# Kernel tuning notes

Measured on AMD Instinct MI355X. Metric: run time of the kernel, lower is better.

The kernel has to match this reference:

```python
import jax, jax.numpy as jnp
import numpy as np

B, L, S, D, H = 4, 1024, 1024, 1024, 16
HD = D // H  # head_dim = 64


def setup_inputs() -> dict:
    key = jax.random.key(0)
    ks = jax.random.split(key, 12)
    s = 1.0 / np.sqrt(D)
    return {
        "query": jax.random.normal(ks[0], (B, L, D), jnp.float32),
        "key": jax.random.normal(ks[1], (B, S, D), jnp.float32),
        "value": jax.random.normal(ks[2], (B, S, D), jnp.float32),
        "key_padding_mask": jax.random.randint(ks[3], (B, S), 0, 2) > 0,
        "Wq": jax.random.normal(ks[4], (D, D), jnp.float32) * s,
        "bq": jnp.zeros((D,), jnp.float32),
        "Wk": jax.random.normal(ks[5], (D, D), jnp.float32) * s,
        "bk": jnp.zeros((D,), jnp.float32),
        "Wv": jax.random.normal(ks[6], (D, D), jnp.float32) * s,
        "bv": jnp.zeros((D,), jnp.float32),
        "Wo": jax.random.normal(ks[7], (D, D), jnp.float32) * s,
        "bo": jnp.zeros((D,), jnp.float32),
    }


def reference(query, key, value, key_padding_mask, Wq, bq, Wk, bk, Wv, bv, Wo, bo):
    bs, tgt, _ = query.shape
    src = key.shape[1]
    # Q/K/V projections (nn.Linear: x @ W.T + b)
    q = query @ Wq.T + bq
    k = key @ Wk.T + bk
    v = value @ Wv.T + bv
    # split heads: (B, T, H, HD)
    q = q.reshape(bs, tgt, H, HD)
    k = k.reshape(bs, src, H, HD)
    v = v.reshape(bs, src, H, HD)
    # scaled dot-product attention with key padding mask (True = masked)
    scale = 1.0 / jnp.sqrt(jnp.asarray(HD, q.dtype))
    scores = jnp.einsum("blhd,bshd->bhls", q, k) * scale  # (B,H,L,S)
    neg_inf = jnp.asarray(-jnp.inf, scores.dtype)
    scores = scores + jnp.where(key_padding_mask[:, None, None, :], neg_inf, 0.0)
    attn = jax.nn.softmax(scores, axis=-1)
    out = jnp.einsum("bhls,bshd->blhd", attn, v).reshape(bs, tgt, D)
    return out @ Wo.T + bo
```

## Files before the change

### kernel.cpp

```cpp
#include <hip/hip_runtime.h>
#include <hip/hip_bf16.h>


typedef __bf16 bf16;
typedef __bf16 bf16x8 __attribute__((ext_vector_type(8)));
typedef float floatx4 __attribute__((ext_vector_type(4)));

#define D_MODEL 1024
#define NHEAD   16
#define HDIM    64
#define BATCH   4
#define SEQ     1024
#define M_ROWS  (BATCH * SEQ)
#define ACT_N   ((size_t)M_ROWS * D_MODEL)
#define W_N     ((size_t)D_MODEL * D_MODEL)
#define SC2     0.18033688011112042f

#define GLD(gp, lp) __builtin_amdgcn_global_load_lds( \
    (__attribute__((address_space(1))) void*)(gp), \
    (__attribute__((address_space(3))) void*)(lp), 16, 0, 0)

__global__ __launch_bounds__(256)
void k_convert_all(const float* __restrict__ a0, const float* __restrict__ a1,
                   const float* __restrict__ a2,
                   const float* __restrict__ w0, const float* __restrict__ w1,
                   const float* __restrict__ w2, const float* __restrict__ w3,
                   bf16* __restrict__ dst,
                   const unsigned* __restrict__ m, float* __restrict__ mbias)
{
    if (blockIdx.x == 8192) {
        __shared__ unsigned viol[4];
        __shared__ int fmsh;
        if (threadIdx.x < 4) viol[threadIdx.x] = 0;
        __syncthreads();
        unsigned a = 0, b = 0, c = 0, d = 0;
        for (int i = threadIdx.x; i < 1024; i += 256) {
            unsigned v = m[i];
            if (v > 1u) a = 1;
            if (((v & 0xFFu) > 1u) || (((v >> 8) & 0xFFu) > 1u) ||
                (((v >> 16) & 0xFFu) > 1u) || (((v >> 24) & 0xFFu) > 1u)) b = 1;
            unsigned lo = v & 0xFFFFu, hi = v >> 16;
            if (!((lo == 0u || lo == 0x3F80u) && (hi == 0u || hi == 0x3F80u))) c = 1;
            if (lo != 0u) d = 1;
        }
        if (a) atomicOr(&viol[0], 1u);
        if (b) atomicOr(&viol[1], 1u);
        if (c) atomicOr(&viol[2], 1u);
        if (d) atomicOr(&viol[3], 1u);
        __syncthreads();
        if (threadIdx.x == 0) {
            int fm;
            if (!viol[0])      fm = 1;
            else if (!viol[1]) fm = 0;
            else if (!viol[2]) fm = viol[3] ? 2 : 3;
            else               fm = 0;
            fmsh = fm;
        }
        __syncthreads();
        const int fm = fmsh;
        for (int i = 0; i < 16; ++i) {
            int s = i * 256 + threadIdx.x;
            bool msk;
            if (fm == 1)      msk = ((const int*)m)[s] != 0;
            else if (fm == 2) msk = ((const unsigned short*)m)[s] != 0;
            else if (fm == 3) msk = ((const unsigned*)m)[s] != 0;
            else              msk = ((const unsigned char*)m)[s] != 0;
            mbias[s] = msk ? -1e30f : 0.f;
        }
        return;
    }

    size_t i = ((size_t)blockIdx.x * 256 + threadIdx.x) * 8;
    const float* src; size_t off;
    if (i < ((size_t)12 << 20)) {
        int z = (int)(i >> 22);
        src = (z == 0) ? a0 : (z == 1) ? a1 : a2;
        off = i & (((size_t)1 << 22) - 1);
    } else {
        size_t r = i - ((size_t)12 << 20);
        int j = (int)(r >> 20);
        src = (j == 0) ? w0 : (j == 1) ? w1 : (j == 2) ? w2 : w3;
        off = r & (((size_t)1 << 20) - 1);
    }
    float4 f0 = ((const float4*)(src + off))[0];
    float4 f1 = ((const float4*)(src + off))[1];
    bf16x8 o;
    o[0] = (bf16)f0.x; o[1] = (bf16)f0.y; o[2] = (bf16)f0.z; o[3] = (bf16)f0.w;
    o[4] = (bf16)f1.x; o[5] = (bf16)f1.y; o[6] = (bf16)f1.z; o[7] = (bf16)f1.w;
    *(bf16x8*)(dst + i) = o;
}

template<typename CT>
__device__ __forceinline__ void gemm8_core(const bf16* __restrict__ A,
                                           const bf16* __restrict__ W,
                                           const float* __restrict__ bias,
                                           CT* __restrict__ C,
                                           int m0, int n0, bool rowBias,
                                           bf16* __restrict__ As0,
                                           bf16* __restrict__ Bs0)
{
    const int t    = threadIdx.x;
    const int lane = t & 63;
    const int w    = t >> 6;
    const int wm   = w >> 2;
    const int wn   = w & 3;
    const int l15  = lane & 15;
    const int quad = lane >> 4;
    const int lx   = l15 & 7;

    floatx4 acc[8][4] = {};

    int srow[2], schk[2], ldso[2];
    #pragma unroll
    for (int j = 0; j < 2; ++j) {
        int i = j * 512 + t;
        srow[j] = i >> 3;
        schk[j] = (i & 7) ^ (srow[j] & 7);
        ldso[j] = (j * 512 + w * 64) * 8;
    }

    #define STAGE_HALF(src, rb, k0s, h, dstbuf) do {                          \
        _Pragma("unroll")                                                     \
        for (int j = 0; j < 2; ++j)                                           \
            GLD((src) + (size_t)((rb) + (h) * 128 + srow[j]) * D_MODEL        \
                    + (k0s) + schk[j] * 8,                                    \
                (dstbuf) + (h) * 8192 + ldso[j]);                             \
    } while (0)

    STAGE_HALF(A, m0, 0, 0, As0);
    STAGE_HALF(A, m0, 0, 1, As0);
    STAGE_HALF(W, n0, 0, 0, Bs0);
    STAGE_HALF(W, n0, 0, 1, Bs0);
    __syncthreads();

    for (int kt = 0; kt < 16; ++kt) {
        const int nk = (kt + 1) * 64;
        const bf16* __restrict__ Ab = As0 + (kt & 1) * 16384;
        const bf16* __restrict__ Bb = Bs0 + (kt & 1) * 16384;
        bf16* __restrict__ An = As0 + ((kt + 1) & 1) * 16384;
        bf16* __restrict__ Bn = Bs0 + ((kt + 1) & 1) * 16384;

        #pragma unroll
        for (int ph = 0; ph < 4; ++ph) {
            const int mq = ph >> 1, nq = ph & 1;

            if (nk < D_MODEL) {
                if (ph == 0)      STAGE_HALF(A, m0, nk, 0, An);
                else if (ph == 1) STAGE_HALF(A, m0, nk, 1, An);
                else if (ph == 2) STAGE_HALF(W, n0, nk, 0, Bn);
                else              STAGE_HALF(W, n0, nk, 1, Bn);
            }

            bf16x8 af[4][2], bfr[2][2];
            #pragma unroll
            for (int ii = 0; ii < 4; ++ii) {
                int row = wm * 128 + mq * 64 + ii * 16 + l15;
                #pragma unroll
                for (int kk = 0; kk < 2; ++kk)
                    af[ii][kk] = *(const bf16x8*)
                        &Ab[row * 64 + (((kk * 4 + quad) ^ lx)) * 8];
            }
            #pragma unroll
            for (int jj = 0; jj < 2; ++jj) {
                int row = wn * 64 + nq * 32 + jj * 16 + l15;
                #pragma unroll
                for (int kk = 0; kk < 2; ++kk)
                    bfr[jj][kk] = *(const bf16x8*)
                        &Bb[row * 64 + (((kk * 4 + quad) ^ lx)) * 8];
            }

            #pragma unroll
            for (int ii = 0; ii < 4; ++ii)
                #pragma unroll
                for (int jj = 0; jj < 2; ++jj)
                    #pragma unroll
                    for (int kk = 0; kk < 2; ++kk)
                        acc[mq * 4 + ii][nq * 2 + jj] =
                            __builtin_amdgcn_mfma_f32_16x16x32_bf16(
                                af[ii][kk], bfr[jj][kk],
                                acc[mq * 4 + ii][nq * 2 + jj], 0, 0, 0);
        }
        __syncthreads();
    }

    #pragma unroll
    for (int i = 0; i < 8; ++i) {
        int rowb = m0 + wm * 128 + i * 16 + quad * 4;
        float bvr[4];
        if (rowBias) {
            #pragma unroll
            for (int r = 0; r < 4; ++r) bvr[r] = bias[rowb + r];
        }
        #pragma unroll
        for (int jf = 0; jf < 4; ++jf) {
            int col = n0 + wn * 64 + jf * 16 + l15;
            float bc = rowBias ? 0.f : bias[col];
            #pragma unroll
            for (int r = 0; r < 4; ++r) {
                float val = acc[i][jf][r] + (rowBias ? bvr[r] : bc);
                C[(size_t)(rowb + r) * D_MODEL + col] = (CT)val;
            }
        }
    }
    #undef STAGE_HALF
}

__global__ __launch_bounds__(512, 2)
void k_gemm_proj(const bf16* __restrict__ cq, const bf16* __restrict__ ck,
                 const bf16* __restrict__ cv,
                 const bf16* __restrict__ cWq, const bf16* __restrict__ cWk,
                 const bf16* __restrict__ cWv,
                 const float* __restrict__ bq, const float* __restrict__ bk,
                 const float* __restrict__ bv,
                 bf16* __restrict__ qproj, bf16* __restrict__ kproj,
                 bf16* __restrict__ vt)
{
    extern __shared__ __align__(16) bf16 smem[];
    bf16* As0 = smem;
    bf16* Bs0 = smem + 32768;

    const int bid = blockIdx.x;
    const int tid = (bid & 7) * 24 + (bid >> 3);
    if (tid < 64) {
        gemm8_core<bf16>(cq, cWq, bq, qproj,
                         (tid >> 2) * 256, (tid & 3) * 256, false, As0, Bs0);
    } else if (tid < 128) {
        int u = tid - 64;
        gemm8_core<bf16>(ck, cWk, bk, kproj,
                         (u >> 2) * 256, (u & 3) * 256, false, As0, Bs0);
    } else {
        int v = tid - 128;
        int b = v >> 4, m = (v >> 2) & 3, n = v & 3;
        gemm8_core<bf16>(cWv, cv + (size_t)b * W_N, bv,
                         vt + (size_t)b * W_N, m * 256, n * 256, true,
                         As0, Bs0);
    }
}

__global__ __launch_bounds__(512, 2)
void k_gemm_o(const bf16* __restrict__ A, const bf16* __restrict__ W,
              const float* __restrict__ bb, float* __restrict__ C)
{
    extern __shared__ __align__(16) bf16 smem[];
    bf16* As0 = smem;
    bf16* Bs0 = smem + 32768;

    const int bid = blockIdx.x;
    const int tid = (bid & 7) * 8 + (bid >> 3);
    gemm8_core<float>(A, W, bb, C, (tid >> 2) * 256, (tid & 3) * 256, false,
                      As0, Bs0);
}

__global__ __launch_bounds__(256)
void k_attn(const bf16* __restrict__ qproj, const bf16* __restrict__ kproj,
            const bf16* __restrict__ vt, const float* __restrict__ mbias_g,
            bf16* __restrict__ ctx)
{
    __shared__ alignas(16) bf16 Kst[2][4096];
    __shared__ alignas(16) bf16 Vst[2][4096];
    __shared__ alignas(16) bf16 Past[4096];

    const int t    = threadIdx.x;
    const int lane = t & 63;
    const int w    = t >> 6;
    const int l15  = lane & 15;
    const int quad = lane >> 4;

    const int b  = blockIdx.x >> 4;
    const int h  = blockIdx.x & 15;
    const int q0 = blockIdx.y * 64;

    #pragma unroll
    for (int kk = 0; kk < 2; ++kk) {
        const bf16* gp = qproj + (size_t)(b * SEQ + q0 + w * 16 + l15) * D_MODEL
                       + h * HDIM + kk * 32 + quad * 8;
        GLD(gp, Past + (w * 2 + kk) * 512);
    }
    #pragma unroll
    for (int i = 0; i < 2; ++i) {
        int f   = w * 2 + i;
        int row = (f >> 1) * 16 + l15;
        int cb  = (f & 1) * 32 + quad * 8;
        GLD(kproj + (size_t)(b * SEQ + row) * D_MODEL + h * HDIM + cb,
            Kst[0] + f * 512);
        GLD(vt + (size_t)(b * 1024 + h * HDIM + row) * D_MODEL + cb,
            Vst[0] + f * 512);
    }
    __syncthreads();

    bf16x8 qf[2];
    #pragma unroll
    for (int kk = 0; kk < 2; ++kk)
        qf[kk] = *(const bf16x8*)&Past[(w * 2 + kk) * 512 + lane * 8];

    bf16x8 ones;
    #pragma unroll
    for (int e = 0; e < 8; ++e) ones[e] = (bf16)1.0f;

    floatx4 o[4] = {};
    floatx4 accl = {};

    const int pbase = w * 1024 + (l15 >> 3) * 128 + quad * 32 + (l15 & 7);
    const float* __restrict__ mbb = mbias_g + b * SEQ;

    int cur = 0;
    for (int s0 = 0; s0 < SEQ; s0 += 64) {
        if (s0 + 64 < SEQ) {
            #pragma unroll
            for (int i = 0; i < 2; ++i) {
                int f   = w * 2 + i;
                int row = (f >> 1) * 16 + l15;
                int cb  = (f & 1) * 32 + quad * 8;
                GLD(kproj + (size_t)(b * SEQ + s0 + 64 + row) * D_MODEL
                        + h * HDIM + cb,
                    Kst[cur ^ 1] + f * 512);
                GLD(vt + (size_t)(b * 1024 + h * HDIM + row) * D_MODEL
                        + s0 + 64 + cb,
                    Vst[cur ^ 1] + f * 512);
            }
        }

        floatx4 s_acc[4] = {};
        #pragma unroll
        for (int j = 0; j < 4; ++j)
            #pragma unroll
            for (int kk = 0; kk < 2; ++kk) {
                bf16x8 kf = *(const bf16x8*)&Kst[cur][(j * 2 + kk) * 512 + lane * 8];
                s_acc[j] = __builtin_amdgcn_mfma_f32_16x16x32_bf16(
                    qf[kk], kf, s_acc[j], 0, 0, 0);
            }

        #pragma unroll
        for (int j = 0; j < 4; ++j) {
            float mb = mbb[s0 + j * 16 + l15];
            #pragma unroll
            for (int r = 0; r < 4; ++r) {
                float p = __builtin_amdgcn_exp2f(fmaf(s_acc[j][r], SC2, mb));
                Past[pbase + (j >> 1) * 512 + (j & 1) * 256 + r * 8] = (bf16)p;
            }
        }
        __builtin_amdgcn_wave_barrier();

        bf16x8 pf[2];
        #pragma unroll
        for (int kk = 0; kk < 2; ++kk)
            pf[kk] = *(const bf16x8*)&Past[w * 1024 + kk * 512 + lane * 8];

        #pragma unroll
        for (int kk = 0; kk < 2; ++kk)
            accl = __builtin_amdgcn_mfma_f32_16x16x32_bf16(pf[kk], ones, accl,
                                                           0, 0, 0);
        #pragma unroll
        for (int j = 0; j < 4; ++j)
            #pragma unroll
            for (int kk = 0; kk < 2; ++kk) {
                bf16x8 vf = *(const bf16x8*)&Vst[cur][(j * 2 + kk) * 512 + lane * 8];
                o[j] = __builtin_amdgcn_mfma_f32_16x16x32_bf16(
                    pf[kk], vf, o[j], 0, 0, 0);
            }

        __syncthreads();
        cur ^= 1;
    }

    float inv[4];
    #pragma unroll
    for (int r = 0; r < 4; ++r) inv[r] = (accl[r] > 0.f) ? 1.f / accl[r] : 0.f;
    #pragma unroll
    for (int j = 0; j < 4; ++j)
        #pragma unroll
        for (int r = 0; r < 4; ++r) {
            int row = q0 + w * 16 + quad * 4 + r;
            int col = h * HDIM + j * 16 + l15;
            ctx[(size_t)(b * SEQ + row) * D_MODEL + col] = (bf16)(o[j][r] * inv[r]);
        }
}

extern "C" void kernel_launch(void* const* d_in, const int* in_sizes, int n_in,
                              void* d_out, int out_size, void* d_ws, size_t ws_size,
                              hipStream_t stream)
{
    char* wsb = (char*)d_ws;
    float* mbias = (float*)wsb;
    bf16* cbase = (bf16*)(wsb + 65536);
    bf16 *cq = cbase, *ck = cq + ACT_N, *cv = ck + ACT_N;
    bf16 *cWq = cv + ACT_N, *cWk = cWq + W_N, *cWv = cWk + W_N, *cWo = cWv + W_N;
    bf16* qproj = cWo + W_N;
    bf16* kproj = qproj + ACT_N;
    bf16* vt    = kproj + ACT_N;
    bf16* ctx   = vt + ACT_N;
    float* out  = (float*)d_out;

    static bool attrset = false;
    if (!attrset) {
        hipFuncSetAttribute((const void*)k_gemm_proj,
                            hipFuncAttributeMaxDynamicSharedMemorySize, 131072);
        hipFuncSetAttribute((const void*)k_gemm_o,
                            hipFuncAttributeMaxDynamicSharedMemorySize, 131072);
        attrset = true;
    }

    k_convert_all<<<8193, 256, 0, stream>>>(
        (const float*)d_in[0], (const float*)d_in[1], (const float*)d_in[2],
        (const float*)d_in[4], (const float*)d_in[6], (const float*)d_in[8],
        (const float*)d_in[10], cbase, (const unsigned*)d_in[3], mbias);

    k_gemm_proj<<<192, 512, 131072, stream>>>(cq, ck, cv, cWq, cWk, cWv,
                                              (const float*)d_in[5],
                                              (const float*)d_in[7],
                                              (const float*)d_in[9],
                                              qproj, kproj, vt);
    k_attn<<<dim3(64, 16), 256, 0, stream>>>(qproj, kproj, vt, mbias, ctx);
    k_gemm_o<<<64, 512, 131072, stream>>>(ctx, cWo, (const float*)d_in[11], out);
}
```

Baseline: 220.7 us.

## Process two query tiles per attention wave and narrow output GEMM tiles

The attention kernel now handles 128 queries per block, with each wave computing two 16-row query groups that share every K and V fragment read from LDS. This halves K/V staging traffic per query and the block count, at the cost of more registers and a larger padded P buffer. The output projection GEMM is templated on a 256x128 tile and launches 128 blocks instead of 64, so more compute units are used, while each block stages a smaller B tile.

```diff
diff --git a/kernel.cpp b/kernel.cpp
--- a/kernel.cpp
+++ b/kernel.cpp
@@ -90,7 +90,7 @@
     *(bf16x8*)(dst + i) = o;
 }
 
-template<typename CT>
+template<typename CT, int NT>
 __device__ __forceinline__ void gemm8_core(const bf16* __restrict__ A,
                                            const bf16* __restrict__ W,
                                            const float* __restrict__ bias,
@@ -108,7 +108,10 @@
     const int quad = lane >> 4;
     const int lx   = l15 & 7;
 
-    floatx4 acc[8][4] = {};
+    constexpr int NJ = NT / 128;
+    constexpr int BSTRIDE = NT * 64;
+
+    floatx4 acc[8][NT / 64] = {};
 
     int srow[2], schk[2], ldso[2];
     #pragma unroll
@@ -130,28 +133,34 @@
     STAGE_HALF(A, m0, 0, 0, As0);
     STAGE_HALF(A, m0, 0, 1, As0);
     STAGE_HALF(W, n0, 0, 0, Bs0);
-    STAGE_HALF(W, n0, 0, 1, Bs0);
+    if constexpr (NT == 256) STAGE_HALF(W, n0, 0, 1, Bs0);
     __syncthreads();
 
     for (int kt = 0; kt < 16; ++kt) {
         const int nk = (kt + 1) * 64;
         const bf16* __restrict__ Ab = As0 + (kt & 1) * 16384;
-        const bf16* __restrict__ Bb = Bs0 + (kt & 1) * 16384;
+        const bf16* __restrict__ Bb = Bs0 + (kt & 1) * BSTRIDE;
         bf16* __restrict__ An = As0 + ((kt + 1) & 1) * 16384;
-        bf16* __restrict__ Bn = Bs0 + ((kt + 1) & 1) * 16384;
+        bf16* __restrict__ Bn = Bs0 + ((kt + 1) & 1) * BSTRIDE;
 
         #pragma unroll
         for (int ph = 0; ph < 4; ++ph) {
             const int mq = ph >> 1, nq = ph & 1;
 
             if (nk < D_MODEL) {
-                if (ph == 0)      STAGE_HALF(A, m0, nk, 0, An);
-                else if (ph == 1) STAGE_HALF(A, m0, nk, 1, An);
-                else if (ph == 2) STAGE_HALF(W, n0, nk, 0, Bn);
-                else              STAGE_HALF(W, n0, nk, 1, Bn);
-            }
-
-            bf16x8 af[4][2], bfr[2][2];
+                if constexpr (NT == 256) {
+                    if (ph == 0)      STAGE_HALF(A, m0, nk, 0, An);
+                    else if (ph == 1) STAGE_HALF(A, m0, nk, 1, An);
+                    else if (ph == 2) STAGE_HALF(W, n0, nk, 0, Bn);
+                    else              STAGE_HALF(W, n0, nk, 1, Bn);
+                } else {
+                    if (ph == 0)      STAGE_HALF(A, m0, nk, 0, An);
+                    else if (ph == 1) STAGE_HALF(A, m0, nk, 1, An);
+                    else if (ph == 2) STAGE_HALF(W, n0, nk, 0, Bn);
+                }
+            }
+
+            bf16x8 af[4][2], bfr[NJ][2];
             #pragma unroll
             for (int ii = 0; ii < 4; ++ii) {
                 int row = wm * 128 + mq * 64 + ii * 16 + l15;
@@ -161,8 +170,8 @@
                         &Ab[row * 64 + (((kk * 4 + quad) ^ lx)) * 8];
             }
             #pragma unroll
-            for (int jj = 0; jj < 2; ++jj) {
-                int row = wn * 64 + nq * 32 + jj * 16 + l15;
+            for (int jj = 0; jj < NJ; ++jj) {
+                int row = wn * (NT / 4) + nq * (NT / 8) + jj * 16 + l15;
                 #pragma unroll
                 for (int kk = 0; kk < 2; ++kk)
                     bfr[jj][kk] = *(const bf16x8*)
@@ -172,13 +181,13 @@
             #pragma unroll
             for (int ii = 0; ii < 4; ++ii)
                 #pragma unroll
-                for (int jj = 0; jj < 2; ++jj)
+                for (int jj = 0; jj < NJ; ++jj)
                     #pragma unroll
                     for (int kk = 0; kk < 2; ++kk)
-                        acc[mq * 4 + ii][nq * 2 + jj] =
+                        acc[mq * 4 + ii][nq * NJ + jj] =
                             __builtin_amdgcn_mfma_f32_16x16x32_bf16(
                                 af[ii][kk], bfr[jj][kk],
-                                acc[mq * 4 + ii][nq * 2 + jj], 0, 0, 0);
+                                acc[mq * 4 + ii][nq * NJ + jj], 0, 0, 0);
         }
         __syncthreads();
     }
@@ -192,8 +201,8 @@
             for (int r = 0; r < 4; ++r) bvr[r] = bias[rowb + r];
         }
         #pragma unroll
-        for (int jf = 0; jf < 4; ++jf) {
-            int col = n0 + wn * 64 + jf * 16 + l15;
+        for (int jf = 0; jf < NT / 64; ++jf) {
+            int col = n0 + wn * (NT / 4) + jf * 16 + l15;
             float bc = rowBias ? 0.f : bias[col];
             #pragma unroll
             for (int r = 0; r < 4; ++r) {
@@ -222,18 +231,18 @@
     const int bid = blockIdx.x;
     const int tid = (bid & 7) * 24 + (bid >> 3);
     if (tid < 64) {
-        gemm8_core<bf16>(cq, cWq, bq, qproj,
-                         (tid >> 2) * 256, (tid & 3) * 256, false, As0, Bs0);
+        gemm8_core<bf16, 256>(cq, cWq, bq, qproj,
+                              (tid >> 2) * 256, (tid & 3) * 256, false, As0, Bs0);
     } else if (tid < 128) {
         int u = tid - 64;
-        gemm8_core<bf16>(ck, cWk, bk, kproj,
-                         (u >> 2) * 256, (u & 3) * 256, false, As0, Bs0);
+        gemm8_core<bf16, 256>(ck, cWk, bk, kproj,
+                              (u >> 2) * 256, (u & 3) * 256, false, As0, Bs0);
     } else {
         int v = tid - 128;
         int b = v >> 4, m = (v >> 2) & 3, n = v & 3;
-        gemm8_core<bf16>(cWv, cv + (size_t)b * W_N, bv,
-                         vt + (size_t)b * W_N, m * 256, n * 256, true,
-                         As0, Bs0);
+        gemm8_core<bf16, 256>(cWv, cv + (size_t)b * W_N, bv,
+                              vt + (size_t)b * W_N, m * 256, n * 256, true,
+                              As0, Bs0);
     }
 }
 
@@ -246,9 +255,9 @@
     bf16* Bs0 = smem + 32768;
 
     const int bid = blockIdx.x;
-    const int tid = (bid & 7) * 8 + (bid >> 3);
-    gemm8_core<float>(A, W, bb, C, (tid >> 2) * 256, (tid & 3) * 256, false,
-                      As0, Bs0);
+    const int tid = (bid & 7) * 16 + (bid >> 3);
+    gemm8_core<float, 128>(A, W, bb, C, (tid >> 3) * 256, (tid & 7) * 128,
+                           false, As0, Bs0);
 }
 
 __global__ __launch_bounds__(256)
@@ -258,7 +267,8 @@
 {
     __shared__ alignas(16) bf16 Kst[2][4096];
     __shared__ alignas(16) bf16 Vst[2][4096];
-    __shared__ alignas(16) bf16 Past[4096];
+    __shared__ alignas(16) bf16 Qst[8192];
+    __shared__ alignas(16) bf16 Past[12800];
 
     const int t    = threadIdx.x;
     const int lane = t & 63;
@@ -268,14 +278,17 @@
 
     const int b  = blockIdx.x >> 4;
     const int h  = blockIdx.x & 15;
-    const int q0 = blockIdx.y * 64;
-
-    #pragma unroll
-    for (int kk = 0; kk < 2; ++kk) {
-        const bf16* gp = qproj + (size_t)(b * SEQ + q0 + w * 16 + l15) * D_MODEL
-                       + h * HDIM + kk * 32 + quad * 8;
-        GLD(gp, Past + (w * 2 + kk) * 512);
-    }
+    const int q0 = blockIdx.y * 128;
+
+    #pragma unroll
+    for (int g = 0; g < 2; ++g)
+        #pragma unroll
+        for (int kk = 0; kk < 2; ++kk) {
+            const bf16* gp = qproj
+                + (size_t)(b * SEQ + q0 + w * 32 + g * 16 + l15) * D_MODEL
+                + h * HDIM + kk * 32 + quad * 8;
+            GLD(gp, Qst + (w * 4 + g * 2 + kk) * 512);
+        }
     #pragma unroll
     for (int i = 0; i < 2; ++i) {
         int f   = w * 2 + i;
@@ -288,19 +301,24 @@
     }
     __syncthreads();
 
-    bf16x8 qf[2];
-    #pragma unroll
-    for (int kk = 0; kk < 2; ++kk)
-        qf[kk] = *(const bf16x8*)&Past[(w * 2 + kk) * 512 + lane * 8];
+    bf16x8 qf[2][2];
+    #pragma unroll
+    for (int g = 0; g < 2; ++g)
+        #pragma unroll
+        for (int kk = 0; kk < 2; ++kk)
+            qf[g][kk] = *(const bf16x8*)&Qst[(w * 4 + g * 2 + kk) * 512 + lane * 8];
 
     bf16x8 ones;
     #pragma unroll
     for (int e = 0; e < 8; ++e) ones[e] = (bf16)1.0f;
 
-    floatx4 o[4] = {};
-    floatx4 accl = {};
-
-    const int pbase = w * 1024 + (l15 >> 3) * 128 + quad * 32 + (l15 & 7);
+    floatx4 o[2][4] = {};
+    floatx4 accl[2] = {};
+
+    const int wrb = w * 3200 + (l15 >> 3) * 200 + (quad >> 1) * 80
+                  + (quad & 1) * 32 + (l15 & 7);
+    const int prb = w * 3200 + quad * 200 + (l15 >> 3) * 80
+                  + (l15 & 7) * 8;
     const float* __restrict__ mbb = mbias_g + b * SEQ;
 
     int cur = 0;
@@ -320,60 +338,82 @@
             }
         }
 
-        floatx4 s_acc[4] = {};
-        #pragma unroll
-        for (int j = 0; j < 4; ++j)
-            #pragma unroll
-            for (int kk = 0; kk < 2; ++kk) {
-                bf16x8 kf = *(const bf16x8*)&Kst[cur][(j * 2 + kk) * 512 + lane * 8];
-                s_acc[j] = __builtin_amdgcn_mfma_f32_16x16x32_bf16(
-                    qf[kk], kf, s_acc[j], 0, 0, 0);
-            }
+        floatx4 s_acc[2][4] = {};
+        #pragma unroll
+        for (int j = 0; j < 4; ++j) {
+            bf16x8 kf0 = *(const bf16x8*)&Kst[cur][(j * 2 + 0) * 512 + lane * 8];
+            bf16x8 kf1 = *(const bf16x8*)&Kst[cur][(j * 2 + 1) * 512 + lane * 8];
+            #pragma unroll
+            for (int g = 0; g < 2; ++g) {
+                s_acc[g][j] = __builtin_amdgcn_mfma_f32_16x16x32_bf16(
+                    qf[g][0], kf0, s_acc[g][j], 0, 0, 0);
+                s_acc[g][j] = __builtin_amdgcn_mfma_f32_16x16x32_bf16(
+                    qf[g][1], kf1, s_acc[g][j], 0, 0, 0);
+            }
+        }
 
         #pragma unroll
         for (int j = 0; j < 4; ++j) {
             float mb = mbb[s0 + j * 16 + l15];
             #pragma unroll
-            for (int r = 0; r < 4; ++r) {
-                float p = __builtin_amdgcn_exp2f(fmaf(s_acc[j][r], SC2, mb));
-                Past[pbase + (j >> 1) * 512 + (j & 1) * 256 + r * 8] = (bf16)p;
-            }
+            for (int g = 0; g < 2; ++g)
+                #pragma unroll
+                for (int r = 0; r < 4; ++r) {
+                    float p = __builtin_amdgcn_exp2f(
+                        fmaf(s_acc[g][j][r], SC2, mb));
+                    Past[wrb + g * 1600 + (j >> 1) * 800 + (j & 1) * 400
+                         + r * 8] = (bf16)p;
+                }
         }
         __builtin_amdgcn_wave_barrier();
 
-        bf16x8 pf[2];
-        #pragma unroll
-        for (int kk = 0; kk < 2; ++kk)
-            pf[kk] = *(const bf16x8*)&Past[w * 1024 + kk * 512 + lane * 8];
-
-        #pragma unroll
-        for (int kk = 0; kk < 2; ++kk)
-            accl = __builtin_amdgcn_mfma_f32_16x16x32_bf16(pf[kk], ones, accl,
-                                                           0, 0, 0);
-        #pragma unroll
-        for (int j = 0; j < 4; ++j)
-            #pragma unroll
-            for (int kk = 0; kk < 2; ++kk) {
-                bf16x8 vf = *(const bf16x8*)&Vst[cur][(j * 2 + kk) * 512 + lane * 8];
-                o[j] = __builtin_amdgcn_mfma_f32_16x16x32_bf16(
-                    pf[kk], vf, o[j], 0, 0, 0);
-            }
+        bf16x8 pf[2][2];
+        #pragma unroll
+        for (int g = 0; g < 2; ++g)
+            #pragma unroll
+            for (int kk = 0; kk < 2; ++kk)
+                pf[g][kk] = *(const bf16x8*)&Past[prb + g * 1600 + kk * 800];
+
+        #pragma unroll
+        for (int g = 0; g < 2; ++g)
+            #pragma unroll
+            for (int kk = 0; kk < 2; ++kk)
+                accl[g] = __builtin_amdgcn_mfma_f32_16x16x32_bf16(
+                    pf[g][kk], ones, accl[g], 0, 0, 0);
+
+        #pragma unroll
+        for (int j = 0; j < 4; ++j) {
+            bf16x8 vf0 = *(const bf16x8*)&Vst[cur][(j * 2 + 0) * 512 + lane * 8];
+            bf16x8 vf1 = *(const bf16x8*)&Vst[cur][(j * 2 + 1) * 512 + lane * 8];
+            #pragma unroll
+            for (int g = 0; g < 2; ++g) {
+                o[g][j] = __builtin_amdgcn_mfma_f32_16x16x32_bf16(
+                    pf[g][0], vf0, o[g][j], 0, 0, 0);
+                o[g][j] = __builtin_amdgcn_mfma_f32_16x16x32_bf16(
+                    pf[g][1], vf1, o[g][j], 0, 0, 0);
+            }
+        }
 
         __syncthreads();
         cur ^= 1;
     }
 
-    float inv[4];
-    #pragma unroll
-    for (int r = 0; r < 4; ++r) inv[r] = (accl[r] > 0.f) ? 1.f / accl[r] : 0.f;
-    #pragma unroll
-    for (int j = 0; j < 4; ++j)
-        #pragma unroll
-        for (int r = 0; r < 4; ++r) {
-            int row = q0 + w * 16 + quad * 4 + r;
-            int col = h * HDIM + j * 16 + l15;
-            ctx[(size_t)(b * SEQ + row) * D_MODEL + col] = (bf16)(o[j][r] * inv[r]);
-        }
+    #pragma unroll
+    for (int g = 0; g < 2; ++g) {
+        float inv[4];
+        #pragma unroll
+        for (int r = 0; r < 4; ++r)
+            inv[r] = (accl[g][r] > 0.f) ? 1.f / accl[g][r] : 0.f;
+        #pragma unroll
+        for (int j = 0; j < 4; ++j)
+            #pragma unroll
+            for (int r = 0; r < 4; ++r) {
+                int row = q0 + w * 32 + g * 16 + quad * 4 + r;
+                int col = h * HDIM + j * 16 + l15;
+                ctx[(size_t)(b * SEQ + row) * D_MODEL + col] =
+                    (bf16)(o[g][j][r] * inv[r]);
+            }
+    }
 }
 
 extern "C" void kernel_launch(void* const* d_in, const int* in_sizes, int n_in,
@@ -410,6 +450,6 @@
                                               (const float*)d_in[7],
                                               (const float*)d_in[9],
                                               qproj, kproj, vt);
-    k_attn<<<dim3(64, 16), 256, 0, stream>>>(qproj, kproj, vt, mbias, ctx);
-    k_gemm_o<<<64, 512, 131072, stream>>>(ctx, cWo, (const float*)d_in[11], out);
-}
+    k_attn<<<dim3(64, 8), 256, 0, stream>>>(qproj, kproj, vt, mbias, ctx);
+    k_gemm_o<<<128, 512, 98304, stream>>>(ctx, cWo, (const float*)d_in[11], out);
+}
```

After: 216.2 us. -2.0%, faster.
